# Optimization experiments

Measured on AMD Instinct MI355X. Metric: run time of the kernel, lower is better.

The kernel has to match this reference:

```python
import jax, jax.numpy as jnp
import numpy as np

B = 16
CH = [128, 256, 512, 1024]
DIM = 128
NH = 8
DEPTH = 4
SPLITS = [64, 16, 4, 1]  # ws*ws for ws in [8,4,2,1]
HS = [64, 32, 16, 8]     # spatial size per scale -> num_blocks = 8 everywhere


def _ln(x, g, b, eps=1e-6):
    m = jnp.mean(x, axis=-1, keepdims=True)
    v = jnp.mean((x - m) ** 2, axis=-1, keepdims=True)
    return (x - m) * jax.lax.rsqrt(v + eps) * g + b


def _atten(x, qkvW, projW):
    # x: (B, nb, nb, N=85, C)  -- NOTE: original code never applies 1/scale, faithful here
    Bx, nb, _, N, C = x.shape
    hd = C // NH
    qkv = (x @ qkvW).reshape(Bx, nb, nb, N, 3, NH, hd)
    qkv = jnp.transpose(qkv, (4, 0, 1, 2, 5, 3, 6))  # (3,B,nb,nb,H,N,hd)
    q, k, v = qkv[0], qkv[1], qkv[2]
    att = jnp.einsum('bijhnd,bijhmd->bijhnm', q, k)
    att = jax.nn.softmax(att, axis=-1)  # reshape in original is a no-op for last-axis softmax
    out = jnp.einsum('bijhnm,bijhmd->bijhnd', att, v)
    out = jnp.transpose(out, (0, 1, 2, 4, 3, 5)).reshape(Bx, nb, nb, N, C)
    return out @ projW


def _forward(xs, fcW, fcb, revW, revb, ln1g, ln1b, ln2g, ln2b, qkvW, projW, fc1W, fc1b, fc2W, fc2b):
    ys = []
    for j, item in enumerate(xs):
        item = item @ fcW[j] + fcb[j]            # -> (B,H,W,DIM)
        Bx, H, W, C = item.shape
        ws = 2 ** (DEPTH - j - 1)
        item = item.reshape(Bx, H // ws, ws, W // ws, ws, C)
        item = jnp.transpose(item, (0, 1, 3, 2, 4, 5))
        item = item.reshape(Bx, H // ws, W // ws, ws * ws, C)
        ys.append(item)
    x = jnp.concatenate(ys, axis=-2)             # (B, nb, nb, 85, DIM)
    # InterTransBlock (num=1), dropout is identity at inference
    h = x
    x = _ln(x, ln1g, ln1b)
    x = _atten(x, qkvW, projW)
    x = h + x
    h = x
    x = _ln(x, ln2g, ln2b)
    x = jax.nn.relu(x @ fc1W + fc1b) @ fc2W + fc2b
    x = h + x
    # split per scale and reverse windowing
    outs = []
    idx = 0
    for j, n in enumerate(SPLITS):
        item = x[:, :, :, idx:idx + n, :]
        idx += n
        Bx, nb, _, N, C = item.shape
        ws = 2 ** (DEPTH - j - 1)
        item = item.reshape(Bx, nb, nb, ws, ws, C)
        item = jnp.transpose(item, (0, 1, 3, 2, 4, 5)).reshape(Bx, nb * ws, nb * ws, C)
        outs.append(item @ revW[j] + revb[j])
    return tuple(outs)


def setup_inputs() -> dict:
    key = jax.random.key(0)
    ks = jax.random.split(key, 20)
    d = {}
    for j in range(4):
        d[f'x{j}'] = jax.random.normal(ks[j], (B, HS[j], HS[j], CH[j]), jnp.float32)
        d[f'fcW{j}'] = jax.random.normal(ks[4 + j], (CH[j], DIM), jnp.float32) * 0.02
        d[f'fcb{j}'] = jnp.zeros((DIM,), jnp.float32)
        d[f'revW{j}'] = jax.random.normal(ks[8 + j], (DIM, CH[j]), jnp.float32) * 0.02
        d[f'revb{j}'] = jnp.zeros((CH[j],), jnp.float32)
    d['ln1g'] = jnp.ones((DIM,), jnp.float32)
    d['ln1b'] = jnp.zeros((DIM,), jnp.float32)
    d['ln2g'] = jnp.ones((DIM,), jnp.float32)
    d['ln2b'] = jnp.zeros((DIM,), jnp.float32)
    d['qkvW'] = jax.random.normal(ks[12], (DIM, 3 * DIM), jnp.float32) * 0.02
    d['projW'] = jax.random.normal(ks[13], (DIM, DIM), jnp.float32) * 0.02
    d['fc1W'] = jax.random.normal(ks[14], (DIM, 4 * DIM), jnp.float32) * 0.02
    d['fc1b'] = jnp.zeros((4 * DIM,), jnp.float32)
    d['fc2W'] = jax.random.normal(ks[15], (4 * DIM, DIM), jnp.float32) * 0.02
    d['fc2b'] = jnp.zeros((DIM,), jnp.float32)
    return d


def reference(x0, x1, x2, x3,
              fcW0, fcb0, fcW1, fcb1, fcW2, fcb2, fcW3, fcb3,
              revW0, revb0, revW1, revb1, revW2, revb2, revW3, revb3,
              ln1g, ln1b, ln2g, ln2b, qkvW, projW, fc1W, fc1b, fc2W, fc2b):
    return _forward([x0, x1, x2, x3],
                    [fcW0, fcW1, fcW2, fcW3], [fcb0, fcb1, fcb2, fcb3],
                    [revW0, revW1, revW2, revW3], [revb0, revb1, revb2, revb3],
                    ln1g, ln1b, ln2g, ln2b, qkvW, projW, fc1W, fc1b, fc2W, fc2b)
```

## Files before the change

kernel.cpp:

```cpp
#include <hip/hip_runtime.h>
#include <hip/hip_bf16.h>

#define NTOK 87040

typedef __attribute__((ext_vector_type(8))) short bf16x8;
typedef __attribute__((ext_vector_type(4))) float f32x4;
typedef __attribute__((ext_vector_type(16))) float f32x16;

#define MFMA __builtin_amdgcn_mfma_f32_16x16x32_bf16
#define MFMA32 __builtin_amdgcn_mfma_f32_32x32x16_bf16

__device__ __forceinline__ unsigned short f2b(float f) {
  unsigned int u; __builtin_memcpy(&u, &f, 4);
  u += 0x7fffu + ((u >> 16) & 1u);
  return (unsigned short)(u >> 16);
}
__device__ __forceinline__ float b2f(short s) {
  unsigned int u = ((unsigned int)(unsigned short)s) << 16;
  float f; __builtin_memcpy(&f, &u, 4);
  return f;
}
__device__ __forceinline__ bf16x8 ldg8(const short* p) { return *(const bf16x8*)p; }
__device__ __forceinline__ f32x16 zero16() {
  f32x16 z;
#pragma unroll
  for (int i = 0; i < 16; i++) z[i] = 0.f;
  return z;
}
__device__ __forceinline__ unsigned int pk2(float lo, float hi) {
  float2 t2; t2.x = lo; t2.y = hi;
  __hip_bfloat162 t = __float22bfloat162_rn(t2);
  unsigned int r; __builtin_memcpy(&r, &t, 4);
  return r;
}
__device__ __forceinline__ uint2 pk4(float a, float b, float c, float d) {
  uint2 r; r.x = pk2(a, b); r.y = pk2(c, d);
  return r;
}
__device__ __forceinline__ bf16x8 ldf8(const float* p) {
  float4 a = *(const float4*)p;
  float4 b = *(const float4*)(p + 4);
  unsigned int w[4] = {pk2(a.x, a.y), pk2(a.z, a.w), pk2(b.x, b.y), pk2(b.z, b.w)};
  bf16x8 o; __builtin_memcpy(&o, w, 16);
  return o;
}

__device__ __forceinline__ int tokmap(int p, int hsShift, int wsShift, int tokOff) {
  int HSm = (1 << hsShift) - 1;
  int w = p & HSm;
  int h = (p >> hsShift) & HSm;
  int b = p >> (2 * hsShift);
  int bi = h >> wsShift, bj = w >> wsShift;
  int wsm = (1 << wsShift) - 1;
  int tt = ((h & wsm) << wsShift) + (w & wsm);
  return ((((b << 3) | bi) << 3) | bj) * 85 + tokOff + tt;
}

struct PrepW {
  const float* src[12];
  short* dst[12];
  int kshift[12];
  int N[12];
  int off[13];
};
__global__ __launch_bounds__(256) void prep_w_kernel(PrepW p) {
  int i = blockIdx.x * 256 + threadIdx.x;
  int s = 0;
#pragma unroll
  for (int t = 0; t < 12; t++) if (i >= p.off[t + 1]) s = t + 1;
  if (s >= 12) return;
  int e = i - p.off[s];
  int K = 1 << p.kshift[s];
  int n = e >> p.kshift[s];
  int k = e & (K - 1);
  p.dst[s][e] = (short)f2b(p.src[s][(size_t)k * p.N[s] + n]);
}

struct FcAllArgs {
  const float* xin[4];
  const short* wt[4];
  const float* bias[4];
  int hsS[4]; int wsS[4]; int tokOff[4]; int chShift[4];
};
__global__ __launch_bounds__(256) void fc_all(
    FcAllArgs A, const float* __restrict__ lng, const float* __restrict__ lnb,
    float* __restrict__ X, short* __restrict__ XB) {
  __shared__ float red[4][16 * 129];
  int bid = blockIdx.x;
  int wv = threadIdx.x >> 6, lane = threadIdx.x & 63;
  int col15 = lane & 15, kg = lane >> 4;

  if (bid >= 576) {
    const float* XIN = A.xin[0];
    const short* Wt = A.wt[0];
    const float* bias = A.bias[0];
    int hsShift = A.hsS[0], wsShift = A.wsS[0], tokOff = A.tokOff[0];
    bf16x8 w[8][4];
#pragma unroll
    for (int nt = 0; nt < 8; nt++)
#pragma unroll
      for (int ks = 0; ks < 4; ks++)
        w[nt][ks] = ldg8(Wt + (size_t)(nt * 16 + col15) * 128 + ks * 32 + kg * 8);
    int t = (bid - 576) * 4 + wv;
    int p0 = t * 16;
    const float* abase = XIN + (size_t)(p0 + col15) * 128 + kg * 8;
    bf16x8 a[4];
#pragma unroll
    for (int ks = 0; ks < 4; ks++) a[ks] = ldf8(abase + ks * 32);
    f32x4 c[8];
#pragma unroll
    for (int nt = 0; nt < 8; nt++) c[nt] = (f32x4){0.f, 0.f, 0.f, 0.f};
#pragma unroll
    for (int nt = 0; nt < 8; nt++)
#pragma unroll
      for (int ks = 0; ks < 4; ks++)
        c[nt] = MFMA(w[nt][ks], a[ks], c[nt], 0, 0, 0);
    float vals[8][4];
#pragma unroll
    for (int nt = 0; nt < 8; nt++) {
      float4 bb = *(const float4*)&bias[nt * 16 + kg * 4];
      vals[nt][0] = c[nt][0] + bb.x; vals[nt][1] = c[nt][1] + bb.y;
      vals[nt][2] = c[nt][2] + bb.z; vals[nt][3] = c[nt][3] + bb.w;
    }
    float s1 = 0.f, s2 = 0.f;
#pragma unroll
    for (int nt = 0; nt < 8; nt++)
#pragma unroll
      for (int r = 0; r < 4; r++) { float v = vals[nt][r]; s1 += v; s2 += v * v; }
    s1 += __shfl_xor(s1, 16); s2 += __shfl_xor(s2, 16);
    s1 += __shfl_xor(s1, 32); s2 += __shfl_xor(s2, 32);
    float mean = s1 * (1.f / 128.f);
    float inv = rsqrtf(s2 * (1.f / 128.f) - mean * mean + 1e-6f);
    size_t row = (size_t)tokmap(p0 + col15, hsShift, wsShift, tokOff) * 128;
#pragma unroll
    for (int nt = 0; nt < 8; nt++) {
      int c0 = nt * 16 + kg * 4;
      float4 g4 = *(const float4*)&lng[c0];
      float4 b4 = *(const float4*)&lnb[c0];
      float4 xs;
      xs.x = vals[nt][0]; xs.y = vals[nt][1]; xs.z = vals[nt][2]; xs.w = vals[nt][3];
      *(float4*)&X[row + c0] = xs;
      *(uint2*)&XB[row + c0] = pk4(
          (vals[nt][0] - mean) * inv * g4.x + b4.x,
          (vals[nt][1] - mean) * inv * g4.y + b4.y,
          (vals[nt][2] - mean) * inv * g4.z + b4.z,
          (vals[nt][3] - mean) * inv * g4.w + b4.w);
    }
    return;
  }

  int lvl, lb;
  if (bid < 64) { lvl = 3; lb = bid; }
  else if (bid < 320) { lvl = 2; lb = bid - 64; }
  else { lvl = 1; lb = bid - 320; }
  const float* XIN = A.xin[lvl];
  const short* Wt = A.wt[lvl];
  const float* bias = A.bias[lvl];
  int CH = 1 << A.chShift[lvl];
  int hsShift = A.hsS[lvl], wsShift = A.wsS[lvl], tokOff = A.tokOff[lvl];

  if (lvl >= 2) {
    int p0 = lb * 16;
    int kb = wv * (CH >> 2);
    const float* abase = XIN + (size_t)(p0 + col15) * CH + kb + kg * 8;
    f32x4 c[8];
#pragma unroll
    for (int nt = 0; nt < 8; nt++) c[nt] = (f32x4){0.f, 0.f, 0.f, 0.f};
    int kiters = CH >> 7;
    for (int ks = 0; ks < kiters; ks++) {
      bf16x8 a = ldf8(abase + ks * 32);
#pragma unroll
      for (int nt = 0; nt < 8; nt++) {
        bf16x8 b = ldg8(Wt + (size_t)(nt * 16 + col15) * CH + kb + ks * 32 + kg * 8);
        c[nt] = MFMA(b, a, c[nt], 0, 0, 0);
      }
    }
#pragma unroll
    for (int nt = 0; nt < 8; nt++)
#pragma unroll
      for (int r = 0; r < 4; r++)
        red[wv][col15 * 129 + nt * 16 + kg * 4 + r] = c[nt][r];
    __syncthreads();
    int tt = wv * 4 + kg;
    float v[8], gv[8], bv[8];
#pragma unroll
    for (int nt = 0; nt < 8; nt++) {
      int col = nt * 16 + col15;
      v[nt] = red[0][tt * 129 + col] + red[1][tt * 129 + col] +
              red[2][tt * 129 + col] + red[3][tt * 129 + col] + bias[col];
      gv[nt] = lng[col]; bv[nt] = lnb[col];
    }
    float s1 = 0.f, s2 = 0.f;
#pragma unroll
    for (int nt = 0; nt < 8; nt++) { s1 += v[nt]; s2 += v[nt] * v[nt]; }
#pragma unroll
    for (int m = 1; m < 16; m <<= 1) { s1 += __shfl_xor(s1, m); s2 += __shfl_xor(s2, m); }
    float mean = s1 * (1.f / 128.f);
    float inv = rsqrtf(s2 * (1.f / 128.f) - mean * mean + 1e-6f);
    size_t row = (size_t)tokmap(p0 + tt, hsShift, wsShift, tokOff) * 128;
#pragma unroll
    for (int nt = 0; nt < 8; nt++) {
      int col = nt * 16 + col15;
      X[row + col] = v[nt];
      XB[row + col] = (short)f2b((v[nt] - mean) * inv * gv[nt] + bv[nt]);
    }
  } else {
    int p0 = lb * 64 + wv * 16;
    const float* abase = XIN + (size_t)(p0 + col15) * CH + kg * 8;
    f32x4 c[8];
#pragma unroll
    for (int nt = 0; nt < 8; nt++) c[nt] = (f32x4){0.f, 0.f, 0.f, 0.f};
    int kiters = CH >> 5;
    for (int ks = 0; ks < kiters; ks++) {
      bf16x8 a = ldf8(abase + ks * 32);
#pragma unroll
      for (int nt = 0; nt < 8; nt++) {
        bf16x8 b = ldg8(Wt + (size_t)(nt * 16 + col15) * CH + ks * 32 + kg * 8);
        c[nt] = MFMA(b, a, c[nt], 0, 0, 0);
      }
    }
    float vals[8][4];
#pragma unroll
    for (int nt = 0; nt < 8; nt++) {
      float4 bb = *(const float4*)&bias[nt * 16 + kg * 4];
#pragma unroll
      for (int r = 0; r < 4; r++) vals[nt][r] = c[nt][r] + ((const float*)&bb)[r];
    }
    float s1 = 0.f, s2 = 0.f;
#pragma unroll
    for (int nt = 0; nt < 8; nt++)
#pragma unroll
      for (int r = 0; r < 4; r++) { float v = vals[nt][r]; s1 += v; s2 += v * v; }
    s1 += __shfl_xor(s1, 16); s2 += __shfl_xor(s2, 16);
    s1 += __shfl_xor(s1, 32); s2 += __shfl_xor(s2, 32);
    float mean = s1 * (1.f / 128.f);
    float inv = rsqrtf(s2 * (1.f / 128.f) - mean * mean + 1e-6f);
    size_t row = (size_t)tokmap(p0 + col15, hsShift, wsShift, tokOff) * 128;
#pragma unroll
    for (int nt = 0; nt < 8; nt++) {
      int c0 = nt * 16 + kg * 4;
      float4 g4 = *(const float4*)&lng[c0];
      float4 b4 = *(const float4*)&lnb[c0];
      float4 xs;
      float n0 = (vals[nt][0] - mean) * inv * g4.x + b4.x;
      float n1 = (vals[nt][1] - mean) * inv * g4.y + b4.y;
      float n2 = (vals[nt][2] - mean) * inv * g4.z + b4.z;
      float n3 = (vals[nt][3] - mean) * inv * g4.w + b4.w;
      xs.x = vals[nt][0]; xs.y = vals[nt][1]; xs.z = vals[nt][2]; xs.w = vals[nt][3];
      *(float4*)&X[row + c0] = xs;
      *(uint2*)&XB[row + c0] = pk4(n0, n1, n2, n3);
    }
  }
}

__global__ __launch_bounds__(256) void qkv_mfma(
    const short* __restrict__ XB, const short* __restrict__ Wt,
    short* __restrict__ QKVH, int ntiles) {
  int wv = threadIdx.x >> 6, lane = threadIdx.x & 63;
  int col15 = lane & 15, kg = lane >> 4;
  bf16x8 w[6][4];
#pragma unroll
  for (int i = 0; i < 6; i++)
#pragma unroll
    for (int ks = 0; ks < 4; ks++)
      w[i][ks] = ldg8(Wt + (size_t)((wv * 6 + i) * 16 + col15) * 128 + ks * 32 + kg * 8);
  for (int t = blockIdx.x; t < ntiles; t += gridDim.x) {
    size_t tok0 = (size_t)t * 32;
    bf16x8 a[2][4];
#pragma unroll
    for (int m = 0; m < 2; m++)
#pragma unroll
      for (int ks = 0; ks < 4; ks++)
        a[m][ks] = ldg8(XB + (tok0 + m * 16 + col15) * 128 + ks * 32 + kg * 8);
    f32x4 acc[6][2];
#pragma unroll
    for (int i = 0; i < 6; i++)
#pragma unroll
      for (int m = 0; m < 2; m++) acc[i][m] = (f32x4){0.f, 0.f, 0.f, 0.f};
#pragma unroll
    for (int i = 0; i < 6; i++)
#pragma unroll
      for (int m = 0; m < 2; m++)
#pragma unroll
        for (int ks = 0; ks < 4; ks++)
          acc[i][m] = MFMA(w[i][ks], a[m][ks], acc[i][m], 0, 0, 0);
#pragma unroll
    for (int i = 0; i < 6; i++) {
      size_t hb = (size_t)(wv * 6 + i) * NTOK;
#pragma unroll
      for (int m = 0; m < 2; m++) {
        size_t tok = tok0 + m * 16 + col15;
        *(uint2*)&QKVH[(hb + tok) * 16 + kg * 4] =
            pk4(acc[i][m][0], acc[i][m][1], acc[i][m][2], acc[i][m][3]);
      }
    }
  }
}

#define PLD 104
__global__ __launch_bounds__(64) void attn_mfma(
    const short* __restrict__ QKVH, short* __restrict__ ATB) {
  int blk = blockIdx.x;
  int h = blk & 7, sb = blk >> 3;
  size_t tok0 = (size_t)sb * 85;
  __shared__ short vT[16 * PLD];
  __shared__ short oT[32 * 24];
  int lane = threadIdx.x;
  int c31 = lane & 31, hh = lane >> 5;
  const short* Qp = QKVH + (size_t)h * NTOK * 16;
  const short* Kp = QKVH + (size_t)(8 + h) * NTOK * 16;
  const short* Vp = QKVH + (size_t)(16 + h) * NTOK * 16;

#pragma unroll
  for (int i = 0; i < 3; i++) {
    int idx = i * 64 + lane;
    if (idx < 170) {
      int m = idx >> 1, half = (idx & 1) << 3;
      bf16x8 v = ldg8(Vp + (tok0 + m) * 16 + half);
#pragma unroll
      for (int j = 0; j < 8; j++) vT[(half + j) * PLD + m] = v[j];
    }
  }
  for (int i = lane; i < 176; i += 64) {
    int d = i / 11, m = 85 + i % 11;
    vT[d * PLD + m] = 0;
  }

  bf16x8 ka[3];
#pragma unroll
  for (int kt = 0; kt < 3; kt++) {
    int tk = kt * 32 + c31; if (tk > 84) tk = 84;
    ka[kt] = ldg8(Kp + (tok0 + tk) * 16 + hh * 8);
  }
  bf16x8 va[6];
  int dm = lane & 15;
#pragma unroll
  for (int ks = 0; ks < 6; ks++)
    va[ks] = *(const bf16x8*)&vT[dm * PLD + ks * 16 + hh * 8];

#pragma unroll
  for (int qt = 0; qt < 3; qt++) {
    int tq = qt * 32 + c31; if (tq > 84) tq = 84;
    bf16x8 qb = ldg8(Qp + (tok0 + tq) * 16 + hh * 8);
    f32x16 s[3];
#pragma unroll
    for (int kt = 0; kt < 3; kt++) s[kt] = zero16();
#pragma unroll
    for (int kt = 0; kt < 3; kt++) s[kt] = MFMA32(ka[kt], qb, s[kt], 0, 0, 0);
#pragma unroll
    for (int r = 0; r < 16; r++) {
      int krow = 64 + (r & 3) + 8 * (r >> 2) + 4 * hh;
      if (krow > 84) s[2][r] = -3e30f;
    }
    float mx = -3e30f;
#pragma unroll
    for (int kt = 0; kt < 3; kt++)
#pragma unroll
      for (int r = 0; r < 16; r++) mx = fmaxf(mx, s[kt][r]);
    mx = fmaxf(mx, __shfl_xor(mx, 32));
    float sum = 0.f;
#pragma unroll
    for (int kt = 0; kt < 3; kt++)
#pragma unroll
      for (int r = 0; r < 16; r++) { float e = __expf(s[kt][r] - mx); s[kt][r] = e; sum += e; }
    sum += __shfl_xor(sum, 32);
    float inv = 1.f / sum;
    bf16x8 pb[6];
#pragma unroll
    for (int ks = 0; ks < 6; ks++) {
      int kt = ks >> 1;
      int b = 8 * (ks & 1);
      unsigned int u0 = pk2(s[kt][b + 0] * inv, s[kt][b + 1] * inv);
      unsigned int u1 = pk2(s[kt][b + 2] * inv, s[kt][b + 3] * inv);
      unsigned int v0 = pk2(s[kt][b + 4] * inv, s[kt][b + 5] * inv);
      unsigned int v1 = pk2(s[kt][b + 6] * inv, s[kt][b + 7] * inv);
      unsigned int u0x = (unsigned int)__shfl_xor((int)u0, 32);
      unsigned int u1x = (unsigned int)__shfl_xor((int)u1, 32);
      unsigned int v0x = (unsigned int)__shfl_xor((int)v0, 32);
      unsigned int v1x = (unsigned int)__shfl_xor((int)v1, 32);
      unsigned int wv[4];
      wv[0] = hh ? v0x : u0;
      wv[1] = hh ? v1x : u1;
      wv[2] = hh ? v0 : u0x;
      wv[3] = hh ? v1 : u1x;
      __builtin_memcpy(&pb[ks], wv, 16);
    }
    f32x16 o = zero16();
#pragma unroll
    for (int ks = 0; ks < 6; ks++) o = MFMA32(va[ks], pb[ks], o, 0, 0, 0);
#pragma unroll
    for (int r = 0; r < 8; r++) {
      int d = (r & 3) + 8 * (r >> 2) + 4 * hh;
      oT[c31 * 24 + d] = (short)f2b(o[r]);
    }
    int tl = lane >> 1, hf = (lane & 1) * 8;
    int tq2 = qt * 32 + tl;
    if (tq2 < 85) {
      bf16x8 ov = *(const bf16x8*)&oT[tl * 24 + hf];
      *(bf16x8*)&ATB[(tok0 + tq2) * 128 + h * 16 + hf] = ov;
    }
  }
}

__global__ __launch_bounds__(256) void proj_mfma(
    const short* __restrict__ ATB, const short* __restrict__ Wt,
    const float* __restrict__ lng, const float* __restrict__ lnb,
    float* __restrict__ X, short* __restrict__ XB) {
  int wid = threadIdx.x >> 6, lane = threadIdx.x & 63;
  int col15 = lane & 15, kg = lane >> 4;
  size_t tok0 = (size_t)blockIdx.x * 64 + wid * 16;
  const short* abase = ATB + (tok0 + col15) * 128 + kg * 8;
  bf16x8 a[4];
#pragma unroll
  for (int ks = 0; ks < 4; ks++) a[ks] = ldg8(abase + ks * 32);
  size_t row = (tok0 + col15) * 128;
  float vals[8][4];
#pragma unroll
  for (int nt = 0; nt < 8; nt++) {
    const short* bbase = Wt + (size_t)(nt * 16 + col15) * 128 + kg * 8;
    f32x4 acc = (f32x4){0.f, 0.f, 0.f, 0.f};
#pragma unroll
    for (int ks = 0; ks < 4; ks++) acc = MFMA(ldg8(bbase + ks * 32), a[ks], acc, 0, 0, 0);
    float4 xr = *(const float4*)&X[row + nt * 16 + kg * 4];
    vals[nt][0] = acc[0] + xr.x; vals[nt][1] = acc[1] + xr.y;
    vals[nt][2] = acc[2] + xr.z; vals[nt][3] = acc[3] + xr.w;
  }
  float s1 = 0.f, s2 = 0.f;
#pragma unroll
  for (int nt = 0; nt < 8; nt++)
#pragma unroll
    for (int r = 0; r < 4; r++) { float v = vals[nt][r]; s1 += v; s2 += v * v; }
  s1 += __shfl_xor(s1, 16); s2 += __shfl_xor(s2, 16);
  s1 += __shfl_xor(s1, 32); s2 += __shfl_xor(s2, 32);
  float mean = s1 * (1.f / 128.f);
  float inv = rsqrtf(s2 * (1.f / 128.f) - mean * mean + 1e-6f);
#pragma unroll
  for (int nt = 0; nt < 8; nt++) {
    int c0 = nt * 16 + kg * 4;
    float4 g4 = *(const float4*)&lng[c0];
    float4 b4 = *(const float4*)&lnb[c0];
    float4 xs;
    xs.x = vals[nt][0]; xs.y = vals[nt][1]; xs.z = vals[nt][2]; xs.w = vals[nt][3];
    *(float4*)&X[row + c0] = xs;
    *(uint2*)&XB[row + c0] = pk4(
        (vals[nt][0] - mean) * inv * g4.x + b4.x,
        (vals[nt][1] - mean) * inv * g4.y + b4.y,
        (vals[nt][2] - mean) * inv * g4.z + b4.z,
        (vals[nt][3] - mean) * inv * g4.w + b4.w);
  }
}

#define HLD 520
__global__ __launch_bounds__(512) void ffu_mfma(
    const short* __restrict__ XB, const short* __restrict__ W1t,
    const float* __restrict__ b1, const short* __restrict__ W2t,
    const float* __restrict__ b2, const float* __restrict__ X,
    short* __restrict__ XBo, int ntiles) {
  __shared__ short Hs[32 * HLD];
  int wv = threadIdx.x >> 6, lane = threadIdx.x & 63;
  int col15 = lane & 15, kg = lane >> 4;
  bf16x8 w2[16];
#pragma unroll
  for (int ks = 0; ks < 16; ks++)
    w2[ks] = ldg8(W2t + (size_t)(wv * 16 + col15) * 512 + ks * 32 + kg * 8);
  float4 b2v = *(const float4*)&b2[wv * 16 + kg * 4];
  for (int t = blockIdx.x; t < ntiles; t += gridDim.x) {
    size_t tok0 = (size_t)t * 32;
    bf16x8 a[2][4];
#pragma unroll
    for (int m = 0; m < 2; m++)
#pragma unroll
      for (int ks = 0; ks < 4; ks++)
        a[m][ks] = ldg8(XB + (tok0 + m * 16 + col15) * 128 + ks * 32 + kg * 8);
    f32x4 acc1[4][2];
#pragma unroll
    for (int nt = 0; nt < 4; nt++)
#pragma unroll
      for (int m = 0; m < 2; m++) acc1[nt][m] = (f32x4){0.f, 0.f, 0.f, 0.f};
#pragma unroll
    for (int nt = 0; nt < 4; nt++)
#pragma unroll
      for (int ks = 0; ks < 4; ks++) {
        bf16x8 w1f = ldg8(W1t + (size_t)(wv * 64 + nt * 16 + col15) * 128 + ks * 32 + kg * 8);
#pragma unroll
        for (int m = 0; m < 2; m++)
          acc1[nt][m] = MFMA(w1f, a[m][ks], acc1[nt][m], 0, 0, 0);
      }
    __syncthreads();
#pragma unroll
    for (int nt = 0; nt < 4; nt++) {
      int c0 = wv * 64 + nt * 16 + kg * 4;
      float4 b1v = *(const float4*)&b1[c0];
#pragma unroll
      for (int m = 0; m < 2; m++) {
        int hrow = m * 16 + col15;
        *(uint2*)&Hs[hrow * HLD + c0] = pk4(
            fmaxf(acc1[nt][m][0] + b1v.x, 0.f), fmaxf(acc1[nt][m][1] + b1v.y, 0.f),
            fmaxf(acc1[nt][m][2] + b1v.z, 0.f), fmaxf(acc1[nt][m][3] + b1v.w, 0.f));
      }
    }
    __syncthreads();
    f32x4 acc2[2];
#pragma unroll
    for (int m = 0; m < 2; m++) acc2[m] = (f32x4){0.f, 0.f, 0.f, 0.f};
#pragma unroll
    for (int ks = 0; ks < 16; ks++)
#pragma unroll
      for (int m = 0; m < 2; m++) {
        bf16x8 hhf = *(const bf16x8*)&Hs[(m * 16 + col15) * HLD + ks * 32 + kg * 8];
        acc2[m] = MFMA(w2[ks], hhf, acc2[m], 0, 0, 0);
      }
#pragma unroll
    for (int m = 0; m < 2; m++) {
      size_t row = (tok0 + m * 16 + col15) * 128;
      int c0 = wv * 16 + kg * 4;
      float4 xr = *(const float4*)&X[row + c0];
      *(uint2*)&XBo[row + c0] = pk4(
          xr.x + acc2[m][0] + b2v.x, xr.y + acc2[m][1] + b2v.y,
          xr.z + acc2[m][2] + b2v.z, xr.w + acc2[m][3] + b2v.w);
    }
  }
}

struct RevArgs {
  const short* wt[4];
  const float* bias[4];
  float* out[4];
  int hsS[4]; int wsS[4]; int tokOff[4];
  int chShift[4];
  int ntcShift[4];
};
__global__ __launch_bounds__(256) void rev_all(RevArgs A, const short* __restrict__ XB) {
  int g = blockIdx.x * 4 + (threadIdx.x >> 6);
  int lane = threadIdx.x & 63, col15 = lane & 15, kg = lane >> 4;
  int lvl, lb;
  if (g < 2048) { lvl = 3; lb = g; }
  else if (g < 6144) { lvl = 2; lb = g - 2048; }
  else if (g < 14336) { lvl = 1; lb = g - 6144; }
  else { lvl = 0; lb = g - 14336; }
  int ntcS = A.ntcShift[lvl];
  int tr = lb >> ntcS, tc = lb & ((1 << ntcS) - 1);
  int CHout = 1 << A.chShift[lvl];
  int p0 = tr * 16, c0 = tc * 32;
  int atok = tokmap(p0 + col15, A.hsS[lvl], A.wsS[lvl], A.tokOff[lvl]);
  const short* abase = XB + (size_t)atok * 128 + kg * 8;
  bf16x8 a[4];
#pragma unroll
  for (int ks = 0; ks < 4; ks++) a[ks] = ldg8(abase + ks * 32);
  const short* Wt = A.wt[lvl];
  const float* bias = A.bias[lvl];
  float* out = A.out[lvl];
  size_t orow = (size_t)(p0 + col15) * CHout;
#pragma unroll
  for (int i = 0; i < 2; i++) {
    int col = c0 + i * 16 + col15;
    const short* bbase = Wt + (size_t)col * 128 + kg * 8;
    f32x4 c = (f32x4){0.f, 0.f, 0.f, 0.f};
#pragma unroll
    for (int ks = 0; ks < 4; ks++) c = MFMA(ldg8(bbase + ks * 32), a[ks], c, 0, 0, 0);
    int cc = c0 + i * 16 + kg * 4;
    float4 b4 = *(const float4*)&bias[cc];
    float4 o;
    o.x = c[0] + b4.x; o.y = c[1] + b4.y; o.z = c[2] + b4.z; o.w = c[3] + b4.w;
    *(float4*)&out[orow + cc] = o;
  }
}

extern "C" void kernel_launch(void* const* d_in, const int* in_sizes, int n_in,
                              void* d_out, int out_size, void* d_ws, size_t ws_size,
                              hipStream_t stream) {
  const float* x[4]; const float* fcW[4]; const float* fcb[4];
  const float* revW[4]; const float* revb[4];
  for (int j = 0; j < 4; j++) {
    x[j]    = (const float*)d_in[j * 5 + 0];
    fcW[j]  = (const float*)d_in[j * 5 + 1];
    fcb[j]  = (const float*)d_in[j * 5 + 2];
    revW[j] = (const float*)d_in[j * 5 + 3];
    revb[j] = (const float*)d_in[j * 5 + 4];
  }
  const float* ln1g = (const float*)d_in[20];
  const float* ln1b = (const float*)d_in[21];
  const float* ln2g = (const float*)d_in[22];
  const float* ln2b = (const float*)d_in[23];
  const float* qkvW = (const float*)d_in[24];
  const float* projW = (const float*)d_in[25];
  const float* fc1W = (const float*)d_in[26];
  const float* fc1b = (const float*)d_in[27];
  const float* fc2W = (const float*)d_in[28];
  const float* fc2b = (const float*)d_in[29];

  float* X    = (float*)d_ws;
  short* QKVH = (short*)(X + (size_t)NTOK * 128);
  short* XB   = QKVH + (size_t)NTOK * 384;
  short* ATB  = XB + (size_t)NTOK * 128;
  short* XIN  = ATB + (size_t)NTOK * 128;
  short* WT   = XIN + (size_t)15728640;

  static const int CH[4] = {128, 256, 512, 1024};
  static const int hsS[4] = {6, 5, 4, 3};
  static const int wsS[4] = {3, 2, 1, 0};
  static const int tokOff[4] = {0, 64, 80, 84};
  static const int chShift[4] = {7, 8, 9, 10};
  static const int fcWtOff[4] = {0, 16384, 49152, 114688};
  static const int revWtOff[4] = {245760, 262144, 294912, 360448};
  const int qkvWtOff = 491520, projWtOff = 540672, fc1WtOff = 557056, fc2WtOff = 622592;

  PrepW pw;
  int cum = 0;
  auto setw = [&](int idx, const float* src, short* dst, int K, int N) {
    pw.src[idx] = src; pw.dst[idx] = dst;
    int ksh = 0; while ((1 << ksh) < K) ksh++;
    pw.kshift[idx] = ksh; pw.N[idx] = N;
    pw.off[idx] = cum; cum += K * N;
  };
  for (int j = 0; j < 4; j++) setw(j, fcW[j], WT + fcWtOff[j], CH[j], 128);
  for (int j = 0; j < 4; j++) setw(4 + j, revW[j], WT + revWtOff[j], 128, CH[j]);
  setw(8, qkvW, WT + qkvWtOff, 128, 384);
  setw(9, projW, WT + projWtOff, 128, 128);
  setw(10, fc1W, WT + fc1WtOff, 128, 512);
  setw(11, fc2W, WT + fc2WtOff, 512, 128);
  pw.off[12] = cum;
  prep_w_kernel<<<2688, 256, 0, stream>>>(pw);

  FcAllArgs fa;
  for (int j = 0; j < 4; j++) {
    fa.xin[j] = x[j];
    fa.wt[j] = WT + fcWtOff[j];
    fa.bias[j] = fcb[j];
    fa.hsS[j] = hsS[j]; fa.wsS[j] = wsS[j];
    fa.tokOff[j] = tokOff[j]; fa.chShift[j] = chShift[j];
  }
  fc_all<<<1600, 256, 0, stream>>>(fa, ln1g, ln1b, X, XB);

  qkv_mfma<<<1024, 256, 0, stream>>>(XB, WT + qkvWtOff, QKVH, NTOK / 32);
  attn_mfma<<<1024 * 8, 64, 0, stream>>>(QKVH, ATB);
  proj_mfma<<<NTOK / 64, 256, 0, stream>>>(ATB, WT + projWtOff, ln2g, ln2b, X, XB);
  ffu_mfma<<<680, 512, 0, stream>>>(XB, WT + fc1WtOff, fc1b, WT + fc2WtOff, fc2b, X, XB, NTOK / 32);

  RevArgs ra;
  float* out = (float*)d_out;
  static const size_t outOffArr[4] = {0, 8388608, 12582912, 14680064};
  static const int ntcShift[4] = {2, 3, 4, 5};
  for (int j = 0; j < 4; j++) {
    ra.wt[j] = WT + revWtOff[j];
    ra.bias[j] = revb[j];
    ra.out[j] = out + outOffArr[j];
    ra.hsS[j] = hsS[j]; ra.wsS[j] = wsS[j]; ra.tokOff[j] = tokOff[j];
    ra.chShift[j] = chShift[j]; ra.ntcShift[j] = ntcShift[j];
  }
  rev_all<<<7680, 256, 0, stream>>>(ra, XB);
}
```

Measured before the change: 285.5 us.

## Restructure FFN kernel to 4 waves with one tile per block grid

The fused MLP kernel drops from 8 to 4 waves per block, and each wave now computes twice as many fc1 and fc2 output columns. The persistent grid-stride loop, which kept W2 fragments in registers, is replaced by one 32-token tile per block, so W2 is reloaded from global/L2 inside the k loop. This removes the per-iteration double barrier and raises occupancy through more, smaller blocks, at the cost of more weight traffic and higher per-wave register use for the accumulators.

```diff
diff --git a/kernel.cpp b/kernel.cpp
--- a/kernel.cpp
+++ b/kernel.cpp
@@ -451,73 +451,78 @@
 }
 
 #define HLD 520
-__global__ __launch_bounds__(512) void ffu_mfma(
+__global__ __launch_bounds__(256) void ffu_mfma(
     const short* __restrict__ XB, const short* __restrict__ W1t,
     const float* __restrict__ b1, const short* __restrict__ W2t,
     const float* __restrict__ b2, const float* __restrict__ X,
-    short* __restrict__ XBo, int ntiles) {
+    short* __restrict__ XBo) {
   __shared__ short Hs[32 * HLD];
   int wv = threadIdx.x >> 6, lane = threadIdx.x & 63;
   int col15 = lane & 15, kg = lane >> 4;
-  bf16x8 w2[16];
-#pragma unroll
-  for (int ks = 0; ks < 16; ks++)
-    w2[ks] = ldg8(W2t + (size_t)(wv * 16 + col15) * 512 + ks * 32 + kg * 8);
-  float4 b2v = *(const float4*)&b2[wv * 16 + kg * 4];
-  for (int t = blockIdx.x; t < ntiles; t += gridDim.x) {
-    size_t tok0 = (size_t)t * 32;
-    bf16x8 a[2][4];
-#pragma unroll
-    for (int m = 0; m < 2; m++)
-#pragma unroll
-      for (int ks = 0; ks < 4; ks++)
-        a[m][ks] = ldg8(XB + (tok0 + m * 16 + col15) * 128 + ks * 32 + kg * 8);
-    f32x4 acc1[4][2];
-#pragma unroll
-    for (int nt = 0; nt < 4; nt++)
-#pragma unroll
-      for (int m = 0; m < 2; m++) acc1[nt][m] = (f32x4){0.f, 0.f, 0.f, 0.f};
-#pragma unroll
-    for (int nt = 0; nt < 4; nt++)
-#pragma unroll
-      for (int ks = 0; ks < 4; ks++) {
-        bf16x8 w1f = ldg8(W1t + (size_t)(wv * 64 + nt * 16 + col15) * 128 + ks * 32 + kg * 8);
-#pragma unroll
-        for (int m = 0; m < 2; m++)
-          acc1[nt][m] = MFMA(w1f, a[m][ks], acc1[nt][m], 0, 0, 0);
-      }
-    __syncthreads();
-#pragma unroll
-    for (int nt = 0; nt < 4; nt++) {
-      int c0 = wv * 64 + nt * 16 + kg * 4;
-      float4 b1v = *(const float4*)&b1[c0];
-#pragma unroll
-      for (int m = 0; m < 2; m++) {
-        int hrow = m * 16 + col15;
-        *(uint2*)&Hs[hrow * HLD + c0] = pk4(
-            fmaxf(acc1[nt][m][0] + b1v.x, 0.f), fmaxf(acc1[nt][m][1] + b1v.y, 0.f),
-            fmaxf(acc1[nt][m][2] + b1v.z, 0.f), fmaxf(acc1[nt][m][3] + b1v.w, 0.f));
-      }
-    }
-    __syncthreads();
-    f32x4 acc2[2];
-#pragma unroll
-    for (int m = 0; m < 2; m++) acc2[m] = (f32x4){0.f, 0.f, 0.f, 0.f};
-#pragma unroll
-    for (int ks = 0; ks < 16; ks++)
-#pragma unroll
-      for (int m = 0; m < 2; m++) {
-        bf16x8 hhf = *(const bf16x8*)&Hs[(m * 16 + col15) * HLD + ks * 32 + kg * 8];
-        acc2[m] = MFMA(w2[ks], hhf, acc2[m], 0, 0, 0);
-      }
+  size_t tok0 = (size_t)blockIdx.x * 32;
+  bf16x8 a[2][4];
+#pragma unroll
+  for (int m = 0; m < 2; m++)
+#pragma unroll
+    for (int ks = 0; ks < 4; ks++)
+      a[m][ks] = ldg8(XB + (tok0 + m * 16 + col15) * 128 + ks * 32 + kg * 8);
+  f32x4 acc1[8][2];
+#pragma unroll
+  for (int nt = 0; nt < 8; nt++)
+#pragma unroll
+    for (int m = 0; m < 2; m++) acc1[nt][m] = (f32x4){0.f, 0.f, 0.f, 0.f};
+#pragma unroll
+  for (int nt = 0; nt < 8; nt++)
+#pragma unroll
+    for (int ks = 0; ks < 4; ks++) {
+      bf16x8 w1f = ldg8(W1t + (size_t)(wv * 128 + nt * 16 + col15) * 128 + ks * 32 + kg * 8);
+#pragma unroll
+      for (int m = 0; m < 2; m++)
+        acc1[nt][m] = MFMA(w1f, a[m][ks], acc1[nt][m], 0, 0, 0);
+    }
+#pragma unroll
+  for (int nt = 0; nt < 8; nt++) {
+    int c0 = wv * 128 + nt * 16 + kg * 4;
+    float4 b1v = *(const float4*)&b1[c0];
+#pragma unroll
+    for (int m = 0; m < 2; m++) {
+      int hrow = m * 16 + col15;
+      *(uint2*)&Hs[hrow * HLD + c0] = pk4(
+          fmaxf(acc1[nt][m][0] + b1v.x, 0.f), fmaxf(acc1[nt][m][1] + b1v.y, 0.f),
+          fmaxf(acc1[nt][m][2] + b1v.z, 0.f), fmaxf(acc1[nt][m][3] + b1v.w, 0.f));
+    }
+  }
+  __syncthreads();
+  f32x4 acc2[2][2];
+#pragma unroll
+  for (int i = 0; i < 2; i++)
+#pragma unroll
+    for (int m = 0; m < 2; m++) acc2[i][m] = (f32x4){0.f, 0.f, 0.f, 0.f};
+#pragma unroll
+  for (int ks = 0; ks < 16; ks++) {
+    bf16x8 w2f[2];
+#pragma unroll
+    for (int i = 0; i < 2; i++)
+      w2f[i] = ldg8(W2t + (size_t)(wv * 32 + i * 16 + col15) * 512 + ks * 32 + kg * 8);
+#pragma unroll
+    for (int m = 0; m < 2; m++) {
+      bf16x8 hhf = *(const bf16x8*)&Hs[(m * 16 + col15) * HLD + ks * 32 + kg * 8];
+#pragma unroll
+      for (int i = 0; i < 2; i++)
+        acc2[i][m] = MFMA(w2f[i], hhf, acc2[i][m], 0, 0, 0);
+    }
+  }
+#pragma unroll
+  for (int i = 0; i < 2; i++) {
+    int c0 = wv * 32 + i * 16 + kg * 4;
+    float4 b2v = *(const float4*)&b2[c0];
 #pragma unroll
     for (int m = 0; m < 2; m++) {
       size_t row = (tok0 + m * 16 + col15) * 128;
-      int c0 = wv * 16 + kg * 4;
       float4 xr = *(const float4*)&X[row + c0];
       *(uint2*)&XBo[row + c0] = pk4(
-          xr.x + acc2[m][0] + b2v.x, xr.y + acc2[m][1] + b2v.y,
-          xr.z + acc2[m][2] + b2v.z, xr.w + acc2[m][3] + b2v.w);
+          xr.x + acc2[i][m][0] + b2v.x, xr.y + acc2[i][m][1] + b2v.y,
+          xr.z + acc2[i][m][2] + b2v.z, xr.w + acc2[i][m][3] + b2v.w);
     }
   }
 }
@@ -635,7 +640,7 @@
   qkv_mfma<<<1024, 256, 0, stream>>>(XB, WT + qkvWtOff, QKVH, NTOK / 32);
   attn_mfma<<<1024 * 8, 64, 0, stream>>>(QKVH, ATB);
   proj_mfma<<<NTOK / 64, 256, 0, stream>>>(ATB, WT + projWtOff, ln2g, ln2b, X, XB);
-  ffu_mfma<<<680, 512, 0, stream>>>(XB, WT + fc1WtOff, fc1b, WT + fc2WtOff, fc2b, X, XB, NTOK / 32);
+  ffu_mfma<<<NTOK / 32, 256, 0, stream>>>(XB, WT + fc1WtOff, fc1b, WT + fc2WtOff, fc2b, X, XB);
 
   RevArgs ra;
   float* out = (float*)d_out;
```

Measured after the change: 323.2 us. 13.2% more time.
